# Kernel optimization log

Measured on AMD Instinct MI355X. Metric: run time of the kernel, lower is better.

## Reference

```python
import jax, jax.numpy as jnp
import numpy as np

L, B, S, D, H, DH, F, W = 4, 4, 1024, 768, 12, 64, 3072, 128
R = 2 * W + 1  # 257 relative positions
EPS = 1e-8


def setup_inputs() -> dict:
    key = jax.random.key(0)
    ks = jax.random.split(key, 12)
    sc = 0.02
    rn = lambda k, shape: (jax.random.normal(k, shape, jnp.float32) * sc)
    return {
        'hidden_states': jax.random.normal(ks[0], (B, S, D), jnp.float32),
        'workspace_states': jax.random.normal(ks[1], (B, 8, D), jnp.float32),
        'attention_mask': jnp.ones((B, S), dtype=bool),
        'wq': rn(ks[2], (L, D, D)),
        'wk': rn(ks[3], (L, D, D)),
        'wv': rn(ks[4], (L, D, D)),
        'pos_q': rn(ks[5], (L, H, DH, R)),
        'pos_k': rn(ks[6], (L, H, DH, R)),
        'wo': rn(ks[7], (L, D, D)),
        'bo': jnp.zeros((L, D), jnp.float32),
        'w1': rn(ks[8], (L, D, F)),
        'b1': jnp.zeros((L, F), jnp.float32),
        'w2': rn(ks[9], (L, F, D)),
        'b2': jnp.zeros((L, D), jnp.float32),
        'ln_g': jnp.ones((L, D), jnp.float32),
        'ln_b': jnp.zeros((L, D), jnp.float32),
    }


def _encoder(hidden_states, workspace_states, attention_mask,
             wq, wk, wv, pos_q, pos_k, wo, bo, w1, b1, w2, b2, ln_g, ln_b):
    mask = attention_mask.astype(bool)
    ii = jnp.arange(S)[:, None]
    jj = jnp.arange(S)[None, :]
    # index = clamp(-(i-j) + w, 0, 2w)  -> relative-position bucket per (i,j)
    rel = jnp.clip(jj - ii + W, 0, 2 * W)            # [S,S] int
    band = jnp.abs(ii - jj) <= W                      # triu(-w) & ~triu(w+1)
    m = band[None, None] & mask[:, None, None, :] & mask[:, None, :, None]
    neg = jnp.finfo(jnp.float32).min
    h = hidden_states
    for l in range(L):
        q = (h @ wq[l]).reshape(B, S, H, DH).transpose(0, 2, 1, 3)  # [B,H,S,d]
        k = (h @ wk[l]).reshape(B, S, H, DH).transpose(0, 2, 1, 3)
        v = (h @ wv[l]).reshape(B, S, H, DH).transpose(0, 2, 1, 3)
        score = jnp.einsum('bhid,bhjd->bhij', q, k)
        qpk = jnp.einsum('bhid,hdr->bhir', q, pos_k[l])  # content-to-position
        kpq = jnp.einsum('bhjd,hdr->bhjr', k, pos_q[l])  # position-to-content
        c2p = qpk[:, :, ii, rel]                          # gather -> [B,H,S,S]
        p2c = jnp.swapaxes(kpq[:, :, ii, rel], -1, -2)    # gather + transpose
        score = score + c2p + p2c + neg * (~m)
        proba = jax.nn.softmax(score, axis=-1)
        ctx = jnp.einsum('bhij,bhjd->bhid', proba, v)
        ctx = ctx.transpose(0, 2, 1, 3).reshape(B, S, D)
        h = h + ctx @ wo[l] + bo[l]
        # shared workspace unit: pass-through (zero hidden update)
        inter = jax.nn.gelu(h @ w1[l] + b1[l], approximate=False)
        h = h + inter @ w2[l] + b2[l]
        mu = jnp.mean(h, axis=-1, keepdims=True)
        var = jnp.var(h, axis=-1, keepdims=True)
        h = (h - mu) / jnp.sqrt(var + EPS) * ln_g[l] + ln_b[l]
    return h


def reference(hidden_states, workspace_states, attention_mask,
              wq, wk, wv, pos_q, pos_k, wo, bo, w1, b1, w2, b2, ln_g, ln_b):
    return _encoder(hidden_states, workspace_states, attention_mask,
                    wq, wk, wv, pos_q, pos_k, wo, bo, w1, b1, w2, b2, ln_g, ln_b)
```

## Files before the change

kernel.cpp:

```cpp
#include <hip/hip_runtime.h>
#include <cstdint>
#include <cstddef>

#define L_ 4
#define B_ 4
#define S_ 1024
#define D_ 768
#define H_ 12
#define DH_ 64
#define F_ 3072
#define W_ 128
#define R_ 257
#define RP2_ 272
#define PTR_ 384

using f32x4 = __attribute__((ext_vector_type(4))) float;
typedef __bf16 bf16x8 __attribute__((ext_vector_type(8)));

#define AS1(p) ((const __attribute__((address_space(1))) void*)(p))
#define AS3(p) ((__attribute__((address_space(3))) void*)(p))

__device__ __forceinline__ float bf2f(ushort u) {
  union { uint32_t i; float f; } x; x.i = ((uint32_t)u) << 16; return x.f;
}
__device__ __forceinline__ ushort f2bf(float f) {
  union { float f; uint32_t i; } x; x.f = f;
  uint32_t r = x.i + 0x7FFFu + ((x.i >> 16) & 1u);
  return (ushort)(r >> 16);
}

__global__ __launch_bounds__(256)
void transpose_cvt(const float* __restrict__ in, ushort* __restrict__ out,
                   int K, int N)
{
  __shared__ float tile[32][33];
  int n0 = blockIdx.x * 32, k0 = blockIdx.y * 32;
  int tx = threadIdx.x & 31, ty = threadIdx.x >> 5;
  #pragma unroll
  for (int r = 0; r < 32; r += 8)
    tile[ty + r][tx] = in[(size_t)(k0 + ty + r) * N + n0 + tx];
  __syncthreads();
  #pragma unroll
  for (int r = 0; r < 32; r += 8)
    out[(size_t)(n0 + ty + r) * K + k0 + tx] = f2bf(tile[tx][ty + r]);
}

__global__ __launch_bounds__(256)
void pos_transpose(const float* __restrict__ pos, ushort* __restrict__ posT)
{
  __shared__ float tile[32][33];
  int lh = blockIdx.x;
  int rt = blockIdx.y;
  int dt = blockIdx.z;
  int tx = threadIdx.x & 31, ty = threadIdx.x >> 5;
  const float* src = pos + (size_t)lh * 64 * R_;
  #pragma unroll
  for (int rr = 0; rr < 32; rr += 8) {
    int d = dt * 32 + ty + rr, r = rt * 32 + tx;
    tile[ty + rr][tx] = (r < R_) ? src[(size_t)d * R_ + r] : 0.f;
  }
  __syncthreads();
  ushort* dst = posT + (size_t)lh * PTR_ * 64;
  #pragma unroll
  for (int rr = 0; rr < 32; rr += 8) {
    int r = rt * 32 + ty + rr, d = dt * 32 + tx;
    dst[(size_t)r * 64 + d] = f2bf(tile[tx][ty + rr]);
  }
}

__global__ __launch_bounds__(256)
void init_h(const float* __restrict__ in, float* __restrict__ h,
            ushort* __restrict__ hbf, int n)
{
  int idx = blockIdx.x * 256 + threadIdx.x;
  if (idx < n) { float v = in[idx]; h[idx] = v; hbf[idx] = f2bf(v); }
}

__global__ __launch_bounds__(256)
void copy_out(const float* __restrict__ h, float* __restrict__ out, int n)
{
  int idx = blockIdx.x * 256 + threadIdx.x;
  if (idx < n) out[idx] = h[idx];
}

template<int EPI>
__global__ __launch_bounds__(256)
void gemm_bt(const ushort* __restrict__ A, const ushort* __restrict__ Bt,
             int M, int N, int K, const float* __restrict__ bias,
             float* __restrict__ resid, ushort* __restrict__ outbf)
{
  __shared__ ushort Asm[128 * 64];
  __shared__ ushort Bsm[128 * 64];
  const int bm = blockIdx.x, bn = blockIdx.y;
  const int tid = threadIdx.x;
  const int lane = tid & 63, w = tid >> 6;
  const int wm = w >> 1, wn = w & 1;
  const int c = lane & 15, g = lane >> 4;
  const size_t rowA0 = (size_t)bm * 128, rowB0 = (size_t)bn * 128;

  const int sr  = lane >> 3;
  const int sc8 = ((lane & 7) ^ sr) * 8;
  const ushort* aSrc = A  + (rowA0 + w * 32 + sr) * (size_t)K + sc8;
  const ushort* bSrc = Bt + (rowB0 + w * 32 + sr) * (size_t)K + sc8;
  const ushort* aDst = Asm + (w * 32) * 64;
  const ushort* bDst = Bsm + (w * 32) * 64;

  f32x4 acc[4][4] = {};

  for (int k0 = 0; k0 < K; k0 += 64) {
    __syncthreads();
    #pragma unroll
    for (int it = 0; it < 4; ++it) {
      __builtin_amdgcn_global_load_lds(AS1(aSrc + (size_t)(it * 8) * K + k0),
                                       AS3(aDst + it * 8 * 64), 16, 0, 0);
      __builtin_amdgcn_global_load_lds(AS1(bSrc + (size_t)(it * 8) * K + k0),
                                       AS3(bDst + it * 8 * 64), 16, 0, 0);
    }
    __syncthreads();

    #pragma unroll
    for (int ks = 0; ks < 2; ++ks) {
      bf16x8 af[4], bfr[4];
      #pragma unroll
      for (int m = 0; m < 4; ++m) {
        int row = wm * 64 + m * 16 + c;
        af[m] = *(const bf16x8*)((const char*)Asm + row * 128 +
                                 ((ks * 64 + g * 16) ^ ((row & 7) << 4)));
      }
      #pragma unroll
      for (int n = 0; n < 4; ++n) {
        int row = wn * 64 + n * 16 + c;
        bfr[n] = *(const bf16x8*)((const char*)Bsm + row * 128 +
                                  ((ks * 64 + g * 16) ^ ((row & 7) << 4)));
      }
      #pragma unroll
      for (int m = 0; m < 4; ++m)
        #pragma unroll
        for (int n = 0; n < 4; ++n)
          acc[m][n] = __builtin_amdgcn_mfma_f32_16x16x32_bf16(
              af[m], bfr[n], acc[m][n], 0, 0, 0);
    }
  }

  const int cr = g * 4, cc = c;
  #pragma unroll
  for (int m = 0; m < 4; ++m) {
    #pragma unroll
    for (int n = 0; n < 4; ++n) {
      #pragma unroll
      for (int q = 0; q < 4; ++q) {
        size_t row = rowA0 + wm * 64 + m * 16 + cr + q;
        size_t col = rowB0 + wn * 64 + n * 16 + cc;
        float v = acc[m][n][q];
        if constexpr (EPI == 0) {
          outbf[row * N + col] = f2bf(v);
        } else if constexpr (EPI == 1) {
          float x = v + bias[col];
          float gl = 0.5f * x * (1.0f + erff(x * 0.70710678118654752f));
          outbf[row * N + col] = f2bf(gl);
        } else if constexpr (EPI == 2) {
          float x = v + bias[col] + resid[row * N + col];
          resid[row * N + col] = x;
          outbf[row * N + col] = f2bf(x);
        } else {
          float x = v + bias[col] + resid[row * N + col];
          resid[row * N + col] = x;
        }
      }
    }
  }
}

__global__ __launch_bounds__(256)
void pos_mfma(const ushort* __restrict__ qkv,
              const ushort* __restrict__ posTq, const ushort* __restrict__ posTk,
              ushort* __restrict__ qpk, ushort* __restrict__ kpq)
{
  __shared__ ushort Asm[128 * 64];
  __shared__ ushort Bsm[128 * 64];
  const int bm = blockIdx.x, bn = blockIdx.y, z = blockIdx.z;
  const int h = z >> 1, which = z & 1;
  const ushort* A  = qkv + (which ? 768 : 0) + h * 64;
  const ushort* Bt = (which ? posTq : posTk) + (size_t)h * PTR_ * 64;
  ushort* out = which ? kpq : qpk;
  const int tid = threadIdx.x, lane = tid & 63, w = tid >> 6;
  const int wm = w >> 1, wn = w & 1;
  const int c = lane & 15, g = lane >> 4;

  #pragma unroll
  for (int it = 0; it < 4; ++it) {
    int row = (tid >> 3) + it * 32;
    int d0 = (tid & 7) * 8;
    uint4 av = *(const uint4*)(A + (size_t)(bm * 128 + row) * 2304 + d0);
    *(uint4*)((char*)Asm + row * 128 + ((d0 * 2) ^ ((row & 7) << 4))) = av;
    uint4 bv = *(const uint4*)(Bt + (size_t)(bn * 128 + row) * 64 + d0);
    *(uint4*)((char*)Bsm + row * 128 + ((d0 * 2) ^ ((row & 7) << 4))) = bv;
  }
  __syncthreads();

  f32x4 acc[4][4] = {};
  #pragma unroll
  for (int ks = 0; ks < 2; ++ks) {
    bf16x8 af[4], bfr[4];
    #pragma unroll
    for (int m = 0; m < 4; ++m) {
      int row = wm * 64 + m * 16 + c;
      af[m] = *(const bf16x8*)((const char*)Asm + row * 128 +
                               ((ks * 64 + g * 16) ^ ((row & 7) << 4)));
    }
    #pragma unroll
    for (int n = 0; n < 4; ++n) {
      int row = wn * 64 + n * 16 + c;
      bfr[n] = *(const bf16x8*)((const char*)Bsm + row * 128 +
                                ((ks * 64 + g * 16) ^ ((row & 7) << 4)));
    }
    #pragma unroll
    for (int m = 0; m < 4; ++m)
      #pragma unroll
      for (int n = 0; n < 4; ++n)
        acc[m][n] = __builtin_amdgcn_mfma_f32_16x16x32_bf16(
            af[m], bfr[n], acc[m][n], 0, 0, 0);
  }

  #pragma unroll
  for (int m = 0; m < 4; ++m) {
    #pragma unroll
    for (int n = 0; n < 4; ++n) {
      #pragma unroll
      for (int q = 0; q < 4; ++q) {
        int rowl = wm * 64 + m * 16 + g * 4 + q;
        int bi = bm * 128 + rowl;
        int b = bi >> 10, i = bi & 1023;
        int col = bn * 128 + wn * 64 + n * 16 + c;
        if (col < RP2_)
          out[((size_t)((b * H_ + h) * S_ + i)) * RP2_ + col] =
              f2bf(acc[m][n][q]);
      }
    }
  }
}

__global__ __launch_bounds__(256)
void attn_mfma(const ushort* __restrict__ qkv,
               const ushort* __restrict__ qpk,
               const ushort* __restrict__ kpq,
               ushort* __restrict__ ctx)
{
  __shared__ ushort Qs[64 * 64];
  __shared__ ushort Ks[64 * 64];
  __shared__ ushort VTs[64 * 64];
  __shared__ ushort Ps[4][16 * 64];

  const int it0 = blockIdx.x;
  const int bh = blockIdx.y;
  const int b = bh / H_, h = bh - b * H_;
  const int i0 = it0 * 64;
  const int tid = threadIdx.x;
  const int lane = tid & 63, w = tid >> 6;
  const int c = lane & 15, g = lane >> 4;
  const size_t qkv_row0 = (size_t)(b * S_) * 2304;

  {
    int rr = tid >> 3, d0 = (tid & 7) * 8;
    #pragma unroll
    for (int it = 0; it < 2; ++it) {
      int row = rr + it * 32;
      uint4 v = *(const uint4*)(qkv + qkv_row0 + (size_t)(i0 + row) * 2304 +
                                h * 64 + d0);
      *(uint4*)((char*)Qs + row * 128 + ((d0 * 2) ^ ((row & 7) << 4))) = v;
    }
  }
  __syncthreads();

  bf16x8 qb[2];
  #pragma unroll
  for (int ks = 0; ks < 2; ++ks) {
    int row = w * 16 + c;
    qb[ks] = *(const bf16x8*)((const char*)Qs + row * 128 +
                              ((ks * 64 + g * 16) ^ ((row & 7) << 4)));
  }

  f32x4 acc[4] = {};
  float mrun = -1e30f, lrun = 0.f;
  const int i_mine = i0 + w * 16 + c;
  const ushort* qrow = qpk + ((size_t)(bh * S_) + i_mine) * RP2_;
  const ushort* kbase = kpq + (size_t)(bh * S_) * RP2_;

  for (int ccnk = 0; ccnk < 5; ++ccnk) {
    int jb = i0 - 128 + 64 * ccnk;
    if (jb < 0 || jb >= S_) continue;
    __syncthreads();
    {
      int rr = tid >> 3, d0 = (tid & 7) * 8;
      #pragma unroll
      for (int it = 0; it < 2; ++it) {
        int row = rr + it * 32;
        const ushort* src = qkv + qkv_row0 + (size_t)(jb + row) * 2304 +
                            768 + h * 64 + d0;
        uint4 kv = *(const uint4*)src;
        *(uint4*)((char*)Ks + row * 128 + ((d0 * 2) ^ ((row & 7) << 4))) = kv;
        uint4 vv = *(const uint4*)(src + 768);
        ushort tmp[8];
        *(uint4*)tmp = vv;
        #pragma unroll
        for (int e = 0; e < 8; ++e) {
          int e2 = (e + tid) & 7;
          int d = d0 + e2;
          *(ushort*)((char*)VTs + d * 128 + ((row * 2) ^ ((d & 7) << 4))) =
              tmp[e2];
        }
      }
    }
    __syncthreads();

    f32x4 sc[4];
    #pragma unroll
    for (int f = 0; f < 4; ++f) {
      f32x4 zz = {0.f, 0.f, 0.f, 0.f};
      #pragma unroll
      for (int ks = 0; ks < 2; ++ks) {
        int row = f * 16 + c;
        bf16x8 a = *(const bf16x8*)((const char*)Ks + row * 128 +
                                    ((ks * 64 + g * 16) ^ ((row & 7) << 4)));
        zz = __builtin_amdgcn_mfma_f32_16x16x32_bf16(a, qb[ks], zz, 0, 0, 0);
      }
      sc[f] = zz;
    }

    float svals[16];
    #pragma unroll
    for (int f = 0; f < 4; ++f) {
      #pragma unroll
      for (int q = 0; q < 4; ++q) {
        int jl = f * 16 + g * 4 + q;
        int j = jb + jl;
        int dlt = j - i_mine;
        float s = sc[f][q];
        if (dlt >= -W_ && dlt <= W_) {
          s += bf2f(qrow[dlt + W_]);
          s += bf2f(kbase[(size_t)j * RP2_ + (W_ - dlt)]);
        } else {
          s = -1e30f;
        }
        svals[f * 4 + q] = s;
      }
    }

    float cm = svals[0];
    #pragma unroll
    for (int q = 1; q < 16; ++q) cm = fmaxf(cm, svals[q]);
    cm = fmaxf(cm, __shfl_xor(cm, 16, 64));
    cm = fmaxf(cm, __shfl_xor(cm, 32, 64));
    float mnew = fmaxf(mrun, cm);
    float cf = __expf(mrun - mnew);
    float psum = 0.f;
    ushort pb[16];
    #pragma unroll
    for (int q = 0; q < 16; ++q) {
      float p = __expf(svals[q] - mnew);
      psum += p;
      pb[q] = f2bf(p);
    }
    psum += __shfl_xor(psum, 16, 64);
    psum += __shfl_xor(psum, 32, 64);
    lrun = lrun * cf + psum;
    mrun = mnew;

    float cfr[4];
    #pragma unroll
    for (int q = 0; q < 4; ++q) cfr[q] = __shfl(cf, (g << 2) + q, 64);
    #pragma unroll
    for (int n = 0; n < 4; ++n)
      #pragma unroll
      for (int q = 0; q < 4; ++q) acc[n][q] *= cfr[q];

    #pragma unroll
    for (int f = 0; f < 4; ++f) {
      uint2 p2;
      p2.x = (uint)pb[f * 4 + 0] | ((uint)pb[f * 4 + 1] << 16);
      p2.y = (uint)pb[f * 4 + 2] | ((uint)pb[f * 4 + 3] << 16);
      *(uint2*)((char*)&Ps[w][0] + c * 128 +
                ((f * 32 + g * 8) ^ ((c & 7) << 4))) = p2;
    }
    asm volatile("s_waitcnt lgkmcnt(0)" ::: "memory");

    #pragma unroll
    for (int ks = 0; ks < 2; ++ks) {
      bf16x8 pa = *(const bf16x8*)((const char*)&Ps[w][0] + c * 128 +
                                   ((ks * 64 + g * 16) ^ ((c & 7) << 4)));
      #pragma unroll
      for (int n = 0; n < 4; ++n) {
        int dd = n * 16 + c;
        bf16x8 bv = *(const bf16x8*)((const char*)VTs + dd * 128 +
                                     ((ks * 64 + g * 16) ^ ((dd & 7) << 4)));
        acc[n] = __builtin_amdgcn_mfma_f32_16x16x32_bf16(pa, bv, acc[n], 0, 0, 0);
      }
    }
  }

  float inv = 1.0f / lrun;
  float invr[4];
  #pragma unroll
  for (int q = 0; q < 4; ++q) invr[q] = __shfl(inv, (g << 2) + q, 64);
  #pragma unroll
  for (int n = 0; n < 4; ++n) {
    #pragma unroll
    for (int q = 0; q < 4; ++q) {
      int i_g = i0 + w * 16 + g * 4 + q;
      int d = n * 16 + c;
      ctx[((size_t)(b * S_ + i_g)) * D_ + h * 64 + d] = f2bf(acc[n][q] * invr[q]);
    }
  }
}

__global__ __launch_bounds__(256)
void ln_kernel(float* __restrict__ h, ushort* __restrict__ hbf,
               const float* __restrict__ g, const float* __restrict__ be)
{
  __shared__ float red[8];
  __shared__ float mv[2];
  int row = blockIdx.x, tid = threadIdx.x;
  float* hr = h + (size_t)row * D_;
  float v0 = hr[tid], v1 = hr[tid + 256], v2 = hr[tid + 512];
  float s = v0 + v1 + v2;
  float s2 = v0 * v0 + v1 * v1 + v2 * v2;
  #pragma unroll
  for (int o = 32; o >= 1; o >>= 1) {
    s += __shfl_xor(s, o, 64);
    s2 += __shfl_xor(s2, o, 64);
  }
  int wave = tid >> 6, lane = tid & 63;
  if (lane == 0) { red[wave] = s; red[4 + wave] = s2; }
  __syncthreads();
  if (tid == 0) {
    float ts = red[0] + red[1] + red[2] + red[3];
    float t2 = red[4] + red[5] + red[6] + red[7];
    float mu = ts / (float)D_;
    float var = t2 / (float)D_ - mu * mu;
    mv[0] = mu; mv[1] = rsqrtf(var + 1e-8f);
  }
  __syncthreads();
  float mu = mv[0], rstd = mv[1];
  #pragma unroll
  for (int cidx = 0; cidx < 3; ++cidx) {
    int col = tid + cidx * 256;
    float v = (cidx == 0) ? v0 : (cidx == 1) ? v1 : v2;
    float x = (v - mu) * rstd * g[col] + be[col];
    hr[col] = x;
    hbf[(size_t)row * D_ + col] = f2bf(x);
  }
}

extern "C" void kernel_launch(void* const* d_in, const int* in_sizes, int n_in,
                              void* d_out, int out_size, void* d_ws, size_t ws_size,
                              hipStream_t stream)
{
  const float* hidden = (const float*)d_in[0];
  const float* wq  = (const float*)d_in[3];
  const float* wk  = (const float*)d_in[4];
  const float* wv  = (const float*)d_in[5];
  const float* pq  = (const float*)d_in[6];
  const float* pk  = (const float*)d_in[7];
  const float* wo  = (const float*)d_in[8];
  const float* bo  = (const float*)d_in[9];
  const float* w1  = (const float*)d_in[10];
  const float* b1  = (const float*)d_in[11];
  const float* w2  = (const float*)d_in[12];
  const float* b2  = (const float*)d_in[13];
  const float* lng = (const float*)d_in[14];
  const float* lnb = (const float*)d_in[15];
  float* out = (float*)d_out;

  char* ws = (char*)d_ws;
  size_t off = 0;
  auto alloc = [&](size_t bytes) {
    void* p = ws + off;
    off += (bytes + 255) & ~(size_t)255;
    return p;
  };
  const size_t NT = (size_t)B_ * S_;
  ushort* wqkv_t = (ushort*)alloc((size_t)L_ * 2304 * 768 * 2);
  ushort* wo_t   = (ushort*)alloc((size_t)L_ * 768 * 768 * 2);
  ushort* w1_t   = (ushort*)alloc((size_t)L_ * 3072 * 768 * 2);
  ushort* w2_t   = (ushort*)alloc((size_t)L_ * 768 * 3072 * 2);
  ushort* posTq  = (ushort*)alloc((size_t)L_ * H_ * PTR_ * 64 * 2);
  ushort* posTk  = (ushort*)alloc((size_t)L_ * H_ * PTR_ * 64 * 2);
  float*  hbuf   = (float*) alloc(NT * D_ * 4);
  ushort* hbf    = (ushort*)alloc(NT * D_ * 2);
  ushort* qkv    = (ushort*)alloc(NT * 2304 * 2);
  ushort* qpk    = (ushort*)alloc((size_t)B_ * H_ * S_ * RP2_ * 2);
  ushort* kpq    = (ushort*)alloc((size_t)B_ * H_ * S_ * RP2_ * 2);
  ushort* ctx    = (ushort*)alloc(NT * D_ * 2);
  ushort* inter  = (ushort*)alloc(NT * F_ * 2);
  (void)ws_size; (void)in_sizes; (void)n_in; (void)out_size;

  for (int l = 0; l < L_; ++l) {
    const size_t dd = (size_t)768 * 768;
    transpose_cvt<<<dim3(24, 24), 256, 0, stream>>>(
        wq + l * dd, wqkv_t + (size_t)l * 2304 * 768, 768, 768);
    transpose_cvt<<<dim3(24, 24), 256, 0, stream>>>(
        wk + l * dd, wqkv_t + (size_t)l * 2304 * 768 + dd, 768, 768);
    transpose_cvt<<<dim3(24, 24), 256, 0, stream>>>(
        wv + l * dd, wqkv_t + (size_t)l * 2304 * 768 + 2 * dd, 768, 768);
    transpose_cvt<<<dim3(24, 24), 256, 0, stream>>>(
        wo + l * dd, wo_t + l * dd, 768, 768);
    transpose_cvt<<<dim3(96, 24), 256, 0, stream>>>(
        w1 + (size_t)l * 768 * 3072, w1_t + (size_t)l * 3072 * 768, 768, 3072);
    transpose_cvt<<<dim3(24, 96), 256, 0, stream>>>(
        w2 + (size_t)l * 3072 * 768, w2_t + (size_t)l * 768 * 3072, 3072, 768);
  }
  pos_transpose<<<dim3(48, 12, 2), 256, 0, stream>>>(pq, posTq);
  pos_transpose<<<dim3(48, 12, 2), 256, 0, stream>>>(pk, posTk);

  init_h<<<(int)((NT * D_ + 255) / 256), 256, 0, stream>>>(
      hidden, hbuf, hbf, (int)(NT * D_));

  for (int l = 0; l < L_; ++l) {
    gemm_bt<0><<<dim3(32, 18), 256, 0, stream>>>(
        hbf, wqkv_t + (size_t)l * 2304 * 768, 4096, 2304, 768,
        nullptr, nullptr, qkv);
    pos_mfma<<<dim3(32, 3, 24), 256, 0, stream>>>(
        qkv, posTq + (size_t)l * H_ * PTR_ * 64,
        posTk + (size_t)l * H_ * PTR_ * 64, qpk, kpq);
    attn_mfma<<<dim3(16, 48), 256, 0, stream>>>(qkv, qpk, kpq, ctx);
    gemm_bt<2><<<dim3(32, 6), 256, 0, stream>>>(
        ctx, wo_t + (size_t)l * 768 * 768, 4096, 768, 768,
        bo + l * 768, hbuf, hbf);
    gemm_bt<1><<<dim3(32, 24), 256, 0, stream>>>(
        hbf, w1_t + (size_t)l * 3072 * 768, 4096, 3072, 768,
        b1 + l * 3072, nullptr, inter);
    gemm_bt<3><<<dim3(32, 6), 256, 0, stream>>>(
        inter, w2_t + (size_t)l * 768 * 3072, 4096, 768, 3072,
        b2 + l * 768, hbuf, nullptr);
    ln_kernel<<<4096, 256, 0, stream>>>(hbuf, hbf, lng + l * 768, lnb + l * 768);
  }

  copy_out<<<(int)((NT * D_ + 255) / 256), 256, 0, stream>>>(
      hbuf, out, (int)(NT * D_));
}
```

Baseline: 1.162 ms.

## Double-buffer LDS tiles in bf16 GEMM to overlap loads with MFMA

The GEMM now keeps two shared-memory tile buffers for A and B. It issues the async global-to-LDS loads for the next K-tile before running the MFMAs on the current one, with one waitcnt and barrier per tile instead of two syncthreads. The aim is to hide global load latency behind matrix math. In exchange, LDS use per block doubles to 64KB, which may reduce occupancy, and the loop assumes an even tile count in K.

Measured after the change: 1.319 ms. 13.5% more time.

```diff
diff --git a/kernel.cpp b/kernel.cpp
--- a/kernel.cpp
+++ b/kernel.cpp
@@ -89,8 +89,8 @@
              int M, int N, int K, const float* __restrict__ bias,
              float* __restrict__ resid, ushort* __restrict__ outbf)
 {
-  __shared__ ushort Asm[128 * 64];
-  __shared__ ushort Bsm[128 * 64];
+  __shared__ ushort Asm[2][128 * 64];
+  __shared__ ushort Bsm[2][128 * 64];
   const int bm = blockIdx.x, bn = blockIdx.y;
   const int tid = threadIdx.x;
   const int lane = tid & 63, w = tid >> 6;
@@ -102,35 +102,34 @@
   const int sc8 = ((lane & 7) ^ sr) * 8;
   const ushort* aSrc = A  + (rowA0 + w * 32 + sr) * (size_t)K + sc8;
   const ushort* bSrc = Bt + (rowB0 + w * 32 + sr) * (size_t)K + sc8;
-  const ushort* aDst = Asm + (w * 32) * 64;
-  const ushort* bDst = Bsm + (w * 32) * 64;
+  const int dstOff = (w * 32) * 64;
 
   f32x4 acc[4][4] = {};
-
-  for (int k0 = 0; k0 < K; k0 += 64) {
-    __syncthreads();
+  const int nt = K >> 6;
+
+  auto STAGE = [&](ushort* Ad, ushort* Bd, int k0) {
     #pragma unroll
     for (int it = 0; it < 4; ++it) {
       __builtin_amdgcn_global_load_lds(AS1(aSrc + (size_t)(it * 8) * K + k0),
-                                       AS3(aDst + it * 8 * 64), 16, 0, 0);
+                                       AS3(Ad + dstOff + it * 8 * 64), 16, 0, 0);
       __builtin_amdgcn_global_load_lds(AS1(bSrc + (size_t)(it * 8) * K + k0),
-                                       AS3(bDst + it * 8 * 64), 16, 0, 0);
-    }
-    __syncthreads();
-
+                                       AS3(Bd + dstOff + it * 8 * 64), 16, 0, 0);
+    }
+  };
+  auto COMPUTE = [&](const ushort* Ab, const ushort* Bb) {
     #pragma unroll
     for (int ks = 0; ks < 2; ++ks) {
       bf16x8 af[4], bfr[4];
       #pragma unroll
       for (int m = 0; m < 4; ++m) {
         int row = wm * 64 + m * 16 + c;
-        af[m] = *(const bf16x8*)((const char*)Asm + row * 128 +
+        af[m] = *(const bf16x8*)((const char*)Ab + row * 128 +
                                  ((ks * 64 + g * 16) ^ ((row & 7) << 4)));
       }
       #pragma unroll
       for (int n = 0; n < 4; ++n) {
         int row = wn * 64 + n * 16 + c;
-        bfr[n] = *(const bf16x8*)((const char*)Bsm + row * 128 +
+        bfr[n] = *(const bf16x8*)((const char*)Bb + row * 128 +
                                   ((ks * 64 + g * 16) ^ ((row & 7) << 4)));
       }
       #pragma unroll
@@ -139,6 +138,25 @@
         for (int n = 0; n < 4; ++n)
           acc[m][n] = __builtin_amdgcn_mfma_f32_16x16x32_bf16(
               af[m], bfr[n], acc[m][n], 0, 0, 0);
+    }
+  };
+
+  STAGE(Asm[0], Bsm[0], 0);
+  asm volatile("s_waitcnt vmcnt(0)" ::: "memory");
+  __builtin_amdgcn_s_barrier();
+
+  for (int t = 0; t < nt; t += 2) {
+    STAGE(Asm[1], Bsm[1], (t + 1) << 6);
+    COMPUTE(Asm[0], Bsm[0]);
+    asm volatile("s_waitcnt vmcnt(0)" ::: "memory");
+    __builtin_amdgcn_s_barrier();
+    if (t + 2 < nt) {
+      STAGE(Asm[0], Bsm[0], (t + 2) << 6);
+      COMPUTE(Asm[1], Bsm[1]);
+      asm volatile("s_waitcnt vmcnt(0)" ::: "memory");
+      __builtin_amdgcn_s_barrier();
+    } else {
+      COMPUTE(Asm[1], Bsm[1]);
     }
   }
 
```
